# Optimization experiments

Measured on AMD Instinct MI355X. Metric: run time of the kernel, lower is better.

Reference implementation:

```python
import jax, jax.numpy as jnp
import numpy as np

N = 8192          # nodes
E = 131072        # edges (avg degree 16)
F_IN = 4          # in_channels
F_HID = 128       # GCNConv output channels (hard-coded in module)
C = 16            # out_channels = number of clusters
EPS = 1e-15


def setup_inputs() -> dict:
    key = jax.random.key(0)
    ks = jax.random.split(key, 6)
    x = jax.random.normal(ks[0], (N, F_IN), dtype=jnp.float32)
    W1 = jax.random.normal(ks[1], (F_IN, F_HID), dtype=jnp.float32) / np.sqrt(F_IN)
    b1 = jax.random.normal(ks[2], (F_HID,), dtype=jnp.float32) * 0.01
    Wp = jax.random.normal(ks[3], (F_HID, C), dtype=jnp.float32) / np.sqrt(F_HID)
    bp = jax.random.normal(ks[4], (C,), dtype=jnp.float32) * 0.01
    edge_index = jax.random.randint(ks[5], (2, E), 0, N, dtype=jnp.int64)
    batch = jnp.zeros((N,), dtype=jnp.int64)  # single graph
    return {"x": x, "W1": W1, "b1": b1, "Wp": Wp, "bp": bp,
            "edge_index": edge_index, "batch": batch}


def gcn_conv(x, edge_index, W, b):
    # PyG GCNConv: add self loops, symmetric D^{-1/2}(A+I)D^{-1/2} normalization.
    src, dst = edge_index[0], edge_index[1]
    h = x @ W                                      # [N, F_HID]
    ones = jnp.ones(src.shape[0], dtype=h.dtype)
    deg = jax.ops.segment_sum(ones, dst, num_segments=N) + 1.0  # +1 self loop
    dinv = jax.lax.rsqrt(deg)
    norm = dinv[src] * dinv[dst]                   # [E]
    agg = jax.ops.segment_sum(h[src] * norm[:, None], dst, num_segments=N)
    agg = agg + h * (dinv * dinv)[:, None]         # self-loop message
    return agg + b


def dmon_pool(x, adj, Wp, bp):
    # x: [1, N, F_HID], adj: [1, N, N]; mask is all-ones (single full graph)
    s = jax.nn.softmax(x @ Wp + bp, axis=-1)       # [1, N, C]
    out = jax.nn.selu(jnp.einsum('bnc,bnf->bcf', s, x))     # [1, C, F_HID]
    out_adj = jnp.einsum('bnc,bnm,bmk->bck', s, adj, s)     # [1, C, C]

    # Spectral (modularity) loss
    deg = adj.sum(axis=1)[..., None]               # column sums, [1, N, 1]
    m = deg.sum(axis=(1, 2)) / 2.0                 # [1]
    ca = jnp.einsum('bnc,bnl->bcl', s, deg)        # [1, C, 1]
    normalizer = jnp.matmul(ca, jnp.swapaxes(ca, 1, 2)) / 2.0 / m[:, None, None]
    spectral = (-jnp.trace(out_adj - normalizer, axis1=1, axis2=2) / 2.0 / m).mean()

    # Orthogonality loss
    ss = jnp.einsum('bnc,bnk->bck', s, s)          # [1, C, C]
    i_s = jnp.eye(C, dtype=s.dtype)
    ss_fro = jnp.sqrt(jnp.sum(ss * ss, axis=(1, 2), keepdims=True))
    diff = ss / ss_fro - i_s / jnp.sqrt(jnp.asarray(C, s.dtype))
    ortho = jnp.sqrt(jnp.sum(diff * diff, axis=(1, 2))).mean()

    # Cluster (collapse) loss
    cluster_size = s.sum(axis=1)                   # [1, C]
    cluster = (jnp.linalg.norm(cluster_size, axis=1) / N
               * jnp.sqrt(jnp.asarray(C, s.dtype)) - 1.0).mean()

    # Fix and normalize coarsened adjacency
    ind = jnp.arange(C)
    out_adj = out_adj.at[:, ind, ind].set(0.0)
    d = jnp.sqrt(out_adj.sum(axis=-1))[:, :, None] + EPS   # [1, C, 1]
    out_adj = out_adj / d / jnp.swapaxes(d, 1, 2)
    return s, out, out_adj, spectral, ortho, cluster


def reference(x, W1, b1, Wp, bp, edge_index, batch):
    h = jax.nn.relu(gcn_conv(x, edge_index, W1, b1))        # [N, 128]
    xd = h[None]                                            # to_dense_batch, B=1
    src, dst = edge_index[0], edge_index[1]
    adj = jnp.zeros((N, N), dtype=h.dtype).at[src, dst].add(1.0)[None]  # to_dense_adj
    s, out, out_adj, sp, o, c = dmon_pool(xd, adj, Wp, bp)
    return jax.nn.log_softmax(out, axis=-1), sp + o + c, s
```

## Files before the change

kernel.cpp:

```cpp
#include <hip/hip_runtime.h>
#include <math.h>

#define NN 8192
#define FH 128
#define NC 16
#define HP 132
#define CHUNK 32

#define WS_CNT   0
#define WS_AGG4  8192
#define WS_ORAW  40960
#define WS_SS    49152
#define WS_CA    50176
#define WS_CS    50432
#define WS_TR    50688
#define WS_END   51200
#define WS_ACC_BEGIN_F4 10240
#define WS_ACC_COUNT_F4 2560

__global__ __launch_bounds__(256) void k_zero_cnt(float4* __restrict__ ws) {
    int i = blockIdx.x * blockDim.x + threadIdx.x;
    if (i < NN / 4) ws[i] = make_float4(0.f, 0.f, 0.f, 0.f);
}

__global__ __launch_bounds__(128) void k_degree(const int* __restrict__ ei,
                                                float* __restrict__ ws, int E) {
    int t = threadIdx.x, b = blockIdx.x;
    if (t < 8)
        reinterpret_cast<float4*>(ws)[NN / 4 + b * 8 + t] =
            make_float4(0.f, 0.f, 0.f, 0.f);
    int e = b * 128 + t;
    if (e < E) atomicAdd(&ws[WS_CNT + ei[E + e]], 1.0f);
}

__global__ __launch_bounds__(128) void k_edge_agg(const int* __restrict__ ei,
                                                  const float* __restrict__ x,
                                                  float* __restrict__ ws, int E) {
    int t = threadIdx.x, b = blockIdx.x;
    if (b < 20) {
        reinterpret_cast<float4*>(ws)[WS_ACC_BEGIN_F4 + b * 128 + t] =
            make_float4(0.f, 0.f, 0.f, 0.f);
    }
    int e = b * 128 + t;
    if (e >= E) return;
    int s = ei[e], d = ei[E + e];
    float di = rsqrtf(ws[WS_CNT + s] + 1.0f);
    float4 xv = reinterpret_cast<const float4*>(x)[s];
    float* agg4 = ws + WS_AGG4;
    atomicAdd(&agg4[d * 4 + 0], di * xv.x);
    atomicAdd(&agg4[d * 4 + 1], di * xv.y);
    atomicAdd(&agg4[d * 4 + 2], di * xv.z);
    atomicAdd(&agg4[d * 4 + 3], di * xv.w);
}

__global__ __launch_bounds__(256) void k_node(const float* __restrict__ x,
                                              const float* __restrict__ W1,
                                              const float* __restrict__ b1,
                                              const float* __restrict__ Wp,
                                              const float* __restrict__ bp,
                                              float* __restrict__ ws,
                                              float* __restrict__ s_out) {
    float* cnt  = ws + WS_CNT;
    float* agg4 = ws + WS_AGG4;
    float* oraw = ws + WS_ORAW;
    float* ssb  = ws + WS_SS;
    float* cab  = ws + WS_CA;
    float* csb  = ws + WS_CS;

    __shared__ float h_lds[CHUNK][HP];
    __shared__ float wpT[NC * HP];
    __shared__ float s_lds[CHUNK][NC];
    __shared__ float z_lds[CHUNK][4];
    __shared__ float c_lds[CHUNK];
    int t = threadIdx.x;
    int b = blockIdx.x;
    int base = b * CHUNK;

    #pragma unroll
    for (int r = 0; r < 8; ++r) {
        int idx = r * 256 + t;
        wpT[(idx & 15) * HP + (idx >> 4)] = Wp[idx];
    }
    if (t < CHUNK) {
        float4 a  = reinterpret_cast<const float4*>(agg4)[base + t];
        float4 xv = reinterpret_cast<const float4*>(x)[base + t];
        float cn = cnt[base + t];
        c_lds[t] = cn;
        float di = rsqrtf(cn + 1.0f);
        z_lds[t][0] = di * fmaf(xv.x, di, a.x);
        z_lds[t][1] = di * fmaf(xv.y, di, a.y);
        z_lds[t][2] = di * fmaf(xv.z, di, a.z);
        z_lds[t][3] = di * fmaf(xv.w, di, a.w);
    }
    __syncthreads();

    int f = t & 127;
    {
        float w0 = W1[f], w1 = W1[128 + f], w2 = W1[256 + f], w3 = W1[384 + f];
        float bb = b1[f];
        int n0 = t >> 7;
        #pragma unroll
        for (int r = 0; r < 16; ++r) {
            int n = n0 + r * 2;
            float v = fmaf(z_lds[n][0], w0, bb);
            v = fmaf(z_lds[n][1], w1, v);
            v = fmaf(z_lds[n][2], w2, v);
            v = fmaf(z_lds[n][3], w3, v);
            h_lds[n][f] = fmaxf(v, 0.0f);
        }
    }
    __syncthreads();

    int c = t & 15, g = t >> 4;
    const float4* wrow = reinterpret_cast<const float4*>(&wpT[c * HP]);
    #pragma unroll
    for (int pass = 0; pass < 2; ++pass) {
        int n = pass * 16 + g;
        const float4* hrow = reinterpret_cast<const float4*>(&h_lds[n][0]);
        float logit = bp[c];
        #pragma unroll 8
        for (int q = 0; q < 32; ++q) {
            float4 hv = hrow[q];
            float4 wv = wrow[q];
            logit = fmaf(hv.x, wv.x, logit);
            logit = fmaf(hv.y, wv.y, logit);
            logit = fmaf(hv.z, wv.z, logit);
            logit = fmaf(hv.w, wv.w, logit);
        }
        float m = logit;
        #pragma unroll
        for (int o = 8; o; o >>= 1) m = fmaxf(m, __shfl_xor(m, o, 16));
        float ex = expf(logit - m);
        float sum = ex;
        #pragma unroll
        for (int o = 8; o; o >>= 1) sum += __shfl_xor(sum, o, 16);
        float sv = ex / sum;
        s_lds[n][c] = sv;
        s_out[(base + n) * NC + c] = sv;
    }
    __syncthreads();

    float acc[8] = {0, 0, 0, 0, 0, 0, 0, 0};
    float acc_ss = 0.0f, acc_ca = 0.0f, acc_cs = 0.0f;
    int ch = t >> 7;
    int cS = t >> 4, kS = t & 15;
    #pragma unroll
    for (int i = 0; i < CHUNK; ++i) {
        float hv = h_lds[i][f];
        const float4* sv = reinterpret_cast<const float4*>(&s_lds[i][0]);
        float4 sa = sv[ch * 2], sb = sv[ch * 2 + 1];
        acc[0] = fmaf(sa.x, hv, acc[0]);
        acc[1] = fmaf(sa.y, hv, acc[1]);
        acc[2] = fmaf(sa.z, hv, acc[2]);
        acc[3] = fmaf(sa.w, hv, acc[3]);
        acc[4] = fmaf(sb.x, hv, acc[4]);
        acc[5] = fmaf(sb.y, hv, acc[5]);
        acc[6] = fmaf(sb.z, hv, acc[6]);
        acc[7] = fmaf(sb.w, hv, acc[7]);
        acc_ss = fmaf(s_lds[i][cS], s_lds[i][kS], acc_ss);
    }
    if (t < NC) {
        #pragma unroll
        for (int i = 0; i < CHUNK; ++i) {
            acc_ca = fmaf(s_lds[i][t], c_lds[i], acc_ca);
            acc_cs += s_lds[i][t];
        }
    }
    int rep = b & 3;
    #pragma unroll
    for (int j = 0; j < 8; ++j)
        atomicAdd(&oraw[rep * 2048 + (ch * 8 + j) * FH + f], acc[j]);
    atomicAdd(&ssb[rep * 256 + cS * NC + kS], acc_ss);
    if (t < NC) {
        int rep16 = b & 15;
        atomicAdd(&cab[rep16 * NC + t], acc_ca);
        atomicAdd(&csb[rep16 * NC + t], acc_cs);
    }
}

__global__ __launch_bounds__(256) void k_adj(const int* __restrict__ ei,
                                             const float* __restrict__ s,
                                             float* __restrict__ ws, int E) {
    float* trb = ws + WS_TR;

    int t = threadIdx.x;
    int b = blockIdx.x;
    int e = b * 256 + t;

    float acc = 0.0f;
    if (e < E) {
        int sN = ei[e], dN = ei[E + e];
        const float4* sr = reinterpret_cast<const float4*>(&s[sN * NC]);
        const float4* dr = reinterpret_cast<const float4*>(&s[dN * NC]);
        float4 a0 = sr[0], a1 = sr[1], a2 = sr[2], a3 = sr[3];
        float4 b0 = dr[0], b1 = dr[1], b2 = dr[2], b3 = dr[3];
        acc = a0.x * b0.x + a0.y * b0.y + a0.z * b0.z + a0.w * b0.w;
        acc = fmaf(a1.x, b1.x, acc); acc = fmaf(a1.y, b1.y, acc);
        acc = fmaf(a1.z, b1.z, acc); acc = fmaf(a1.w, b1.w, acc);
        acc = fmaf(a2.x, b2.x, acc); acc = fmaf(a2.y, b2.y, acc);
        acc = fmaf(a2.z, b2.z, acc); acc = fmaf(a2.w, b2.w, acc);
        acc = fmaf(a3.x, b3.x, acc); acc = fmaf(a3.y, b3.y, acc);
        acc = fmaf(a3.z, b3.z, acc); acc = fmaf(a3.w, b3.w, acc);
    }
    #pragma unroll
    for (int o = 32; o; o >>= 1) acc += __shfl_xor(acc, o, 64);
    if ((t & 63) == 0) {
        int wave = (b * 256 + t) >> 6;
        atomicAdd(&trb[(wave & 15) * 32], acc);
    }
}

__device__ __forceinline__ float selu_f(float x) {
    const float a = 1.6732632423543772f, sc = 1.0507009873554805f;
    return sc * (x > 0.0f ? x : a * (expf(x) - 1.0f));
}

__global__ __launch_bounds__(256) void k_final(float* __restrict__ ws,
                                               float* __restrict__ d_out, float Ef) {
    float* oraw = ws + WS_ORAW;
    float* ssb  = ws + WS_SS;
    float* cab  = ws + WS_CA;
    float* csb  = ws + WS_CS;
    float* trb  = ws + WS_TR;
    int t = threadIdx.x;
    int lane = t & 63, w = t >> 6;

    if (w == 0) {
        float tot[4];
        float fr2 = 0.f;
        #pragma unroll
        for (int j = 0; j < 4; ++j) {
            int i = lane + j * 64;
            float v = ssb[i] + ssb[256 + i] + ssb[512 + i] + ssb[768 + i];
            tot[j] = v;
            fr2 += v * v;
        }
        #pragma unroll
        for (int o = 32; o; o >>= 1) fr2 += __shfl_xor(fr2, o, 64);
        float fro = sqrtf(fr2);
        float o2 = 0.f;
        #pragma unroll
        for (int j = 0; j < 4; ++j) {
            int i = lane + j * 64;
            float d = tot[j] / fro - ((i % 17 == 0) ? 0.25f : 0.f);
            o2 += d * d;
        }
        #pragma unroll
        for (int o = 32; o; o >>= 1) o2 += __shfl_xor(o2, o, 64);
        float ortho = sqrtf(o2);

        float tv = 0.f, ca = 0.f, cs = 0.f;
        if (lane < 16) {
            tv = trb[lane * 32];
            #pragma unroll
            for (int r = 0; r < 16; ++r) { ca += cab[r * 16 + lane]; cs += csb[r * 16 + lane]; }
        }
        float tr = tv, can = ca * ca, csn = cs * cs;
        #pragma unroll
        for (int o = 32; o; o >>= 1) {
            tr  += __shfl_xor(tr, o, 64);
            can += __shfl_xor(can, o, 64);
            csn += __shfl_xor(csn, o, 64);
        }
        float spectral = -(tr - can / Ef) / Ef;
        float cluster = sqrtf(csn) / (float)NN * 4.0f - 1.0f;
        if (lane == 0) d_out[NC * FH] = spectral + ortho + cluster;
    }

    #pragma unroll
    for (int rr = 0; rr < 4; ++rr) {
        int cR = w + rr * 4;
        int c0 = lane * 2;
        float va = 0.f, vb = 0.f;
        #pragma unroll
        for (int r = 0; r < 4; ++r) {
            float2 vv = *reinterpret_cast<const float2*>(&oraw[r * 2048 + cR * FH + c0]);
            va += vv.x;
            vb += vv.y;
        }
        va = selu_f(va);
        vb = selu_f(vb);
        float mx = fmaxf(va, vb);
        #pragma unroll
        for (int o = 32; o; o >>= 1) mx = fmaxf(mx, __shfl_xor(mx, o, 64));
        float sm = expf(va - mx) + expf(vb - mx);
        #pragma unroll
        for (int o = 32; o; o >>= 1) sm += __shfl_xor(sm, o, 64);
        float ls = mx + logf(sm);
        d_out[cR * FH + c0]     = va - ls;
        d_out[cR * FH + c0 + 1] = vb - ls;
    }
}

extern "C" void kernel_launch(void* const* d_in, const int* in_sizes, int n_in,
                              void* d_out, int out_size, void* d_ws, size_t ws_size,
                              hipStream_t stream) {
    const float* x  = (const float*)d_in[0];
    const float* W1 = (const float*)d_in[1];
    const float* b1 = (const float*)d_in[2];
    const float* Wp = (const float*)d_in[3];
    const float* bp = (const float*)d_in[4];
    const int*   ei = (const int*)d_in[5];
    int E = in_sizes[5] / 2;

    float* ws  = (float*)d_ws;
    float* out = (float*)d_out;
    float* s   = out + NC * FH + 1;

    k_zero_cnt<<<8, 256, 0, stream>>>((float4*)d_ws);
    k_degree  <<<(E + 127) / 128, 128, 0, stream>>>(ei, ws, E);
    k_edge_agg<<<(E + 127) / 128, 128, 0, stream>>>(ei, x, ws, E);
    k_node    <<<NN / CHUNK, 256, 0, stream>>>(x, W1, b1, Wp, bp, ws, s);
    k_adj     <<<(E + 255) / 256, 256, 0, stream>>>(ei, s, ws, E);
    k_final   <<<1, 256, 0, stream>>>(ws, out, (float)E);
}
```

Measured before the change: 66.30 us.

## Build CSR by destination and gather neighbor features instead of float atomics

Replaces the float-atomic scatter of normalized input features with a CSR construction: an integer degree count, a single-block prefix scan producing offsets and dinv, and a fill pass that places source indices into per-destination slots. k_node then gathers each node's neighbors with 8 lanes per node and a shuffle reduction. The aim is to remove four float atomics per edge. In exchange it adds a kernel launch, a serial single-block scan and an integer atomic per edge in the fill pass. The cnt buffer now holds ints, so any later kernel still reading it as float would be wrong.

```diff
diff --git a/kernel.cpp b/kernel.cpp
--- a/kernel.cpp
+++ b/kernel.cpp
@@ -8,49 +8,73 @@
 #define CHUNK 32
 
 #define WS_CNT   0
-#define WS_AGG4  8192
-#define WS_ORAW  40960
-#define WS_SS    49152
-#define WS_CA    50176
-#define WS_CS    50432
-#define WS_TR    50688
-#define WS_END   51200
-#define WS_ACC_BEGIN_F4 10240
+#define WS_OFF   8192
+#define WS_CUR   16448
+#define WS_DINV  24640
+#define WS_CSRC  32832
+#define WS_ORAW  163904
+#define WS_SS    172096
+#define WS_CA    173120
+#define WS_CS    173376
+#define WS_TR    173632
+#define WS_END   174144
+#define WS_ACC_BEGIN_F4 40976
 #define WS_ACC_COUNT_F4 2560
 
-__global__ __launch_bounds__(256) void k_zero_cnt(float4* __restrict__ ws) {
+__global__ __launch_bounds__(256) void k_zero(float4* __restrict__ ws) {
     int i = blockIdx.x * blockDim.x + threadIdx.x;
-    if (i < NN / 4) ws[i] = make_float4(0.f, 0.f, 0.f, 0.f);
-}
-
-__global__ __launch_bounds__(128) void k_degree(const int* __restrict__ ei,
-                                                float* __restrict__ ws, int E) {
-    int t = threadIdx.x, b = blockIdx.x;
-    if (t < 8)
-        reinterpret_cast<float4*>(ws)[NN / 4 + b * 8 + t] =
-            make_float4(0.f, 0.f, 0.f, 0.f);
-    int e = b * 128 + t;
-    if (e < E) atomicAdd(&ws[WS_CNT + ei[E + e]], 1.0f);
-}
-
-__global__ __launch_bounds__(128) void k_edge_agg(const int* __restrict__ ei,
-                                                  const float* __restrict__ x,
-                                                  float* __restrict__ ws, int E) {
-    int t = threadIdx.x, b = blockIdx.x;
-    if (b < 20) {
-        reinterpret_cast<float4*>(ws)[WS_ACC_BEGIN_F4 + b * 128 + t] =
-            make_float4(0.f, 0.f, 0.f, 0.f);
-    }
-    int e = b * 128 + t;
+    if (i < 2048) ws[i] = make_float4(0.f, 0.f, 0.f, 0.f);
+    else if (i < 2048 + WS_ACC_COUNT_F4)
+        ws[WS_ACC_BEGIN_F4 + (i - 2048)] = make_float4(0.f, 0.f, 0.f, 0.f);
+}
+
+__global__ __launch_bounds__(128) void k_count(const int* __restrict__ ei,
+                                               float* __restrict__ ws, int E) {
+    int* cnt = (int*)(ws + WS_CNT);
+    int e = blockIdx.x * 128 + threadIdx.x;
+    if (e < E) atomicAdd(&cnt[ei[E + e]], 1);
+}
+
+__global__ __launch_bounds__(256) void k_prefix(float* __restrict__ ws) {
+    int* cnt  = (int*)(ws + WS_CNT);
+    int* off  = (int*)(ws + WS_OFF);
+    int* cur  = (int*)(ws + WS_CUR);
+    float* dinv = ws + WS_DINV;
+    __shared__ int psum[256];
+    int t = threadIdx.x;
+    int base = t * 32;
+    int local[32];
+    int sum = 0;
+    #pragma unroll
+    for (int k = 0; k < 32; ++k) { local[k] = cnt[base + k]; sum += local[k]; }
+    psum[t] = sum;
+    __syncthreads();
+    for (int o = 1; o < 256; o <<= 1) {
+        int v = (t >= o) ? psum[t - o] : 0;
+        __syncthreads();
+        psum[t] += v;
+        __syncthreads();
+    }
+    int run = psum[t] - sum;
+    #pragma unroll
+    for (int k = 0; k < 32; ++k) {
+        off[base + k] = run;
+        cur[base + k] = run;
+        dinv[base + k] = rsqrtf((float)local[k] + 1.0f);
+        run += local[k];
+    }
+    if (t == 255) off[NN] = run;
+}
+
+__global__ __launch_bounds__(128) void k_fill(const int* __restrict__ ei,
+                                              float* __restrict__ ws, int E) {
+    int* cur  = (int*)(ws + WS_CUR);
+    int* csrc = (int*)(ws + WS_CSRC);
+    int e = blockIdx.x * 128 + threadIdx.x;
     if (e >= E) return;
     int s = ei[e], d = ei[E + e];
-    float di = rsqrtf(ws[WS_CNT + s] + 1.0f);
-    float4 xv = reinterpret_cast<const float4*>(x)[s];
-    float* agg4 = ws + WS_AGG4;
-    atomicAdd(&agg4[d * 4 + 0], di * xv.x);
-    atomicAdd(&agg4[d * 4 + 1], di * xv.y);
-    atomicAdd(&agg4[d * 4 + 2], di * xv.z);
-    atomicAdd(&agg4[d * 4 + 3], di * xv.w);
+    int slot = atomicAdd(&cur[d], 1);
+    csrc[slot] = s;
 }
 
 __global__ __launch_bounds__(256) void k_node(const float* __restrict__ x,
@@ -60,8 +84,10 @@
                                               const float* __restrict__ bp,
                                               float* __restrict__ ws,
                                               float* __restrict__ s_out) {
-    float* cnt  = ws + WS_CNT;
-    float* agg4 = ws + WS_AGG4;
+    int*   cnti = (int*)(ws + WS_CNT);
+    int*   off  = (int*)(ws + WS_OFF);
+    int*   csrc = (int*)(ws + WS_CSRC);
+    float* dinv = ws + WS_DINV;
     float* oraw = ws + WS_ORAW;
     float* ssb  = ws + WS_SS;
     float* cab  = ws + WS_CA;
@@ -81,16 +107,37 @@
         int idx = r * 256 + t;
         wpT[(idx & 15) * HP + (idx >> 4)] = Wp[idx];
     }
-    if (t < CHUNK) {
-        float4 a  = reinterpret_cast<const float4*>(agg4)[base + t];
-        float4 xv = reinterpret_cast<const float4*>(x)[base + t];
-        float cn = cnt[base + t];
-        c_lds[t] = cn;
-        float di = rsqrtf(cn + 1.0f);
-        z_lds[t][0] = di * fmaf(xv.x, di, a.x);
-        z_lds[t][1] = di * fmaf(xv.y, di, a.y);
-        z_lds[t][2] = di * fmaf(xv.z, di, a.z);
-        z_lds[t][3] = di * fmaf(xv.w, di, a.w);
+
+    {
+        int i = t >> 3, j = t & 7;
+        int o0 = off[base + i], o1 = off[base + i + 1];
+        float ax = 0.f, ay = 0.f, az = 0.f, aw = 0.f;
+        for (int slot = o0 + j; slot < o1; slot += 8) {
+            int sN = csrc[slot];
+            float di = dinv[sN];
+            float4 xv = reinterpret_cast<const float4*>(x)[sN];
+            ax = fmaf(xv.x, di, ax);
+            ay = fmaf(xv.y, di, ay);
+            az = fmaf(xv.z, di, az);
+            aw = fmaf(xv.w, di, aw);
+        }
+        #pragma unroll
+        for (int o = 4; o; o >>= 1) {
+            ax += __shfl_down(ax, o, 8);
+            ay += __shfl_down(ay, o, 8);
+            az += __shfl_down(az, o, 8);
+            aw += __shfl_down(aw, o, 8);
+        }
+        if (j == 0) {
+            float cn = (float)cnti[base + i];
+            c_lds[i] = cn;
+            float dn = dinv[base + i];
+            float4 xv = reinterpret_cast<const float4*>(x)[base + i];
+            z_lds[i][0] = dn * fmaf(xv.x, dn, ax);
+            z_lds[i][1] = dn * fmaf(xv.y, dn, ay);
+            z_lds[i][2] = dn * fmaf(xv.z, dn, az);
+            z_lds[i][3] = dn * fmaf(xv.w, dn, aw);
+        }
     }
     __syncthreads();
 
@@ -307,10 +354,11 @@
     float* out = (float*)d_out;
     float* s   = out + NC * FH + 1;
 
-    k_zero_cnt<<<8, 256, 0, stream>>>((float4*)d_ws);
-    k_degree  <<<(E + 127) / 128, 128, 0, stream>>>(ei, ws, E);
-    k_edge_agg<<<(E + 127) / 128, 128, 0, stream>>>(ei, x, ws, E);
-    k_node    <<<NN / CHUNK, 256, 0, stream>>>(x, W1, b1, Wp, bp, ws, s);
-    k_adj     <<<(E + 255) / 256, 256, 0, stream>>>(ei, s, ws, E);
-    k_final   <<<1, 256, 0, stream>>>(ws, out, (float)E);
-}
+    k_zero  <<<18, 256, 0, stream>>>((float4*)d_ws);
+    k_count <<<(E + 127) / 128, 128, 0, stream>>>(ei, ws, E);
+    k_prefix<<<1, 256, 0, stream>>>(ws);
+    k_fill  <<<(E + 127) / 128, 128, 0, stream>>>(ei, ws, E);
+    k_node  <<<NN / CHUNK, 256, 0, stream>>>(x, W1, b1, Wp, bp, ws, s);
+    k_adj   <<<(E + 255) / 256, 256, 0, stream>>>(ei, s, ws, E);
+    k_final <<<1, 256, 0, stream>>>(ws, out, (float)E);
+}
```

After: 53.74 us, median of 2. 1.23x faster.
